# Kernel tuning notes

Measured on AMD Instinct MI355X. Metric: run time of the kernel, lower is better.

The kernel has to match this reference:

```python
import jax, jax.numpy as jnp
import numpy as np

B = 2048


def _maxpool2(x):
    return jax.lax.reduce_window(x, -jnp.inf, jax.lax.max,
                                 (1, 1, 2, 2), (1, 1, 2, 2), 'VALID')


def setup_inputs() -> dict:
    key = jax.random.key(0)
    ks = jax.random.split(key, 7)
    return {
        'x': jax.random.normal(ks[0], (B, 3, 32, 32), dtype=jnp.float32),
        'conv_w': jax.random.normal(ks[1], (45, 1, 5, 5), dtype=jnp.float32),
        'conv_b': jax.random.normal(ks[2], (45,), dtype=jnp.float32) * 0.1,
        'tree_w': jax.random.normal(ks[3], (1, 16, 15, 3, 7, 7, 2, 2), dtype=jnp.float32),
        'tree_b': jax.random.normal(ks[4], (1, 16, 3, 7), dtype=jnp.float32),
        'fc_w': jax.random.normal(ks[5], (10, 336), dtype=jnp.float32),
        'fc_b': jax.random.normal(ks[6], (10,), dtype=jnp.float32) * 0.1,
    }


def reference(x, conv_w, conv_b, tree_w, tree_b, fc_w, fc_b):
    # grouped conv: in=3, groups=3, out=45, kernel 5x5, VALID -> (B,45,28,28)
    out = jax.lax.conv_general_dilated(
        x, conv_w, window_strides=(1, 1), padding='VALID',
        dimension_numbers=('NCHW', 'OIHW', 'NCHW'), feature_group_count=3)
    out = jax.nn.sigmoid(out + conv_b[None, :, None, None])
    out = _maxpool2(out)  # (B,45,14,14)
    b = out.shape[0]
    # unfold((2,2),stride=2) + the torch reshape/transpose chain is equivalent to:
    # (B,45,14,14) -> (b, g=3, m=15, i=7, ki=2, j=7, kj=2) -> (b,m,g,i,j,ki,kj)
    xt = out.reshape(b, 3, 15, 7, 2, 7, 2).transpose(0, 2, 1, 3, 5, 4, 6)
    # TreeLayer: elementwise mul with weights (16,m,g,i,j,ki,kj) then sum over m,j,ki,kj
    t = jnp.einsum('bmgijkl,fmgijkl->bfgi', xt, tree_w[0]) + tree_b  # (B,16,3,7)
    t = jax.nn.sigmoid(t)
    return t.reshape(b, 16 * 3 * 7) @ fc_w.T + fc_b  # (B,10)
```

## Files before the change

kernel.cpp:

```cpp
#include <hip/hip_runtime.h>
#include <hip/hip_fp16.h>

#define BATCH 2048

typedef _Float16 f16x8 __attribute__((ext_vector_type(8)));
typedef float f32x4 __attribute__((ext_vector_type(4)));

#define RST 36
#define CST 1168
#define IMS 4672
#define IST 448
#define PIS 3152

__device__ __forceinline__ float fast_sigmoid(float v) {
    return __builtin_amdgcn_rcpf(1.0f + __builtin_amdgcn_exp2f(v * -1.44269504f));
}

#define WS_W3B  0
#define WS_FCW  301056

__global__ __launch_bounds__(256) void k_prep(
    const float* __restrict__ tree_w,
    const float* __restrict__ fc_w,
    ushort* __restrict__ W3B,
    float* __restrict__ FCW2,
    float* __restrict__ out)
{
    int pidx = blockIdx.x * 256 + threadIdx.x;
    if (pidx < 35280) {
        float4 v = ((const float4*)tree_w)[pidx];
        int j  = pidx % 7;
        int t1 = pidx / 7;
        int i  = t1 % 7;
        int t2 = t1 / 7;
        int g  = t2 % 3;
        int t3 = t2 / 3;
        int nn = t3 % 15;
        int f  = t3 / 15;
        int gi = g * 7 + i;
        int u  = nn & 7;
        int hi = nn >> 3;
        float vv[4] = {v.x, v.y, v.z, v.w};
        #pragma unroll
        for (int e = 0; e < 4; e++) {
            int ki = e >> 1, kj = e & 1;
            int u27 = ki * 14 + j * 2 + kj;
            int c   = u27 >> 1;
            int qq  = (u27 & 1) * 2 + hi;
            W3B[(size_t)(gi * 14 + c) * 512 + (qq * 16 + f) * 8 + u] =
                __half_as_ushort(__float2half(vv[e]));
        }
    } else if (pidx < 38640) {
        int jj = pidx - 35280;
        int f = jj & 15;
        int r = jj >> 4;
        int i = r % 7;
        int r2 = r / 7;
        int o = r2 % 10;
        int g = r2 / 10;
        FCW2[jj] = fc_w[o * 336 + f * 21 + g * 7 + i];
    } else if (pidx < 48048) {
        int z = pidx - 38640;
        int f  = z & 15;
        int qq = ((z >> 4) & 1) * 2 + 1;
        int r  = z >> 5;
        int c  = r % 14;
        int gi = r / 14;
        W3B[(size_t)(gi * 14 + c) * 512 + (qq * 16 + f) * 8 + 7] = 0;
    } else if (pidx < 68528) {
        out[pidx - 48048] = 0.f;
    }
}

__global__ __launch_bounds__(256, 3) void kF_all(
    const float* __restrict__ x,
    const float* __restrict__ conv_w,
    const float* __restrict__ conv_b,
    const ushort* __restrict__ W3B,
    const float* __restrict__ FCW2,
    const float* __restrict__ tree_b,
    const float* __restrict__ fc_b,
    float* __restrict__ out)
{
    __shared__ __align__(16) ushort xsc[2 * IMS];
    __shared__ __align__(16) ushort ps[4 * PIS];
    __shared__ __align__(16) ushort tsl[28 * 16];

    const int tid  = threadIdx.x;
    const int blk  = blockIdx.x;
    const int quad = blk / 3;
    const int g    = blk - quad * 3;
    const int img0 = quad * 4;
    const int lane = tid & 63;
    const int n    = lane & 15;
    const int q    = lane >> 4;
    const int wave = tid >> 6;

    float4 xv[4];
    #pragma unroll
    for (int im = 0; im < 4; im++)
        xv[im] = ((const float4*)(x + (size_t)(img0 + im) * 3072 + g * 1024))[tid];

    f16x8 B1 = {0, 0, 0, 0, 0, 0, 0, 0};
    f16x8 B2 = {0, 0, 0, 0, 0, 0, 0, 0};
    float bs = 0.f;
    if (n < 15) {
        const float* wrow = conv_w + (g * 15 + n) * 25;
        #pragma unroll
        for (int u = 0; u < 5; u++) B1[u] = (_Float16)wrow[q * 5 + u];
        if (q == 0) {
            #pragma unroll
            for (int u = 0; u < 5; u++) B2[u] = (_Float16)wrow[20 + u];
        }
        bs = conv_b[g * 15 + n] * -1.44269504f;
    }

    const int dr = (n >> 1) & 1, dc = n & 1, n4 = n >> 2;
    const int a2c = (4 - q) * RST;
    int aoff[13], svr[13];
    #pragma unroll
    for (int it = 0; it < 13; it++) {
        int t = wave + it * 4;
        int pb = t * 4 + n4;
        int ph = pb / 14, pw = pb - ph * 14;
        int r = 2 * ph + dr, c = 2 * pw + dc;
        int s = c & 3;
        aoff[it] = s * CST + (r + q) * RST + (c - s);
        int i = t / 7, tt = t - i * 7;
        svr[it] = i * IST + tt * 64 + lane;
    }

    auto conv_tile2 = [&](int it, ushort* pso) {
        const ushort* pA0 = xsc + aoff[it];
        const ushort* pA1 = pA0 + IMS;
        union U { struct { uint2 a, b; } u; f16x8 v; };
        U A1a, A2a, A1b, A2b;
        A1a.u.a = *(const uint2*)pA0;
        A1a.u.b = *(const uint2*)(pA0 + 4);
        A2a.u.a = *(const uint2*)(pA0 + a2c);
        A2a.u.b = *(const uint2*)(pA0 + a2c + 4);
        A1b.u.a = *(const uint2*)pA1;
        A1b.u.b = *(const uint2*)(pA1 + 4);
        A2b.u.a = *(const uint2*)(pA1 + a2c);
        A2b.u.b = *(const uint2*)(pA1 + a2c + 4);
        f32x4 da = {0.f, 0.f, 0.f, 0.f}, db = {0.f, 0.f, 0.f, 0.f};
        da = __builtin_amdgcn_mfma_f32_16x16x32_f16(A1a.v, B1, da, 0, 0, 0);
        db = __builtin_amdgcn_mfma_f32_16x16x32_f16(A1b.v, B1, db, 0, 0, 0);
        da = __builtin_amdgcn_mfma_f32_16x16x32_f16(A2a.v, B2, da, 0, 0, 0);
        db = __builtin_amdgcn_mfma_f32_16x16x32_f16(A2b.v, B2, db, 0, 0, 0);
        float mxa = fmaxf(fmaxf(da[0], da[1]), fmaxf(da[2], da[3]));
        float mxb = fmaxf(fmaxf(db[0], db[1]), fmaxf(db[2], db[3]));
        float ea = __builtin_amdgcn_exp2f(fmaf(mxa, -1.44269504f, bs));
        float eb = __builtin_amdgcn_exp2f(fmaf(mxb, -1.44269504f, bs));
        pso[svr[it]] =
            __half_as_ushort(__float2half(__builtin_amdgcn_rcpf(1.0f + ea)));
        pso[PIS + svr[it]] =
            __half_as_ushort(__float2half(__builtin_amdgcn_rcpf(1.0f + eb)));
    };

    const int row = tid >> 3, colg = (tid & 7) * 4;
    #pragma unroll
    for (int r2 = 0; r2 < 2; r2++) {
        #pragma unroll
        for (int im2 = 0; im2 < 2; im2++) {
            float4 v = xv[r2 * 2 + im2];
            __half2 a = __float22half2_rn(make_float2(v.x, v.y));
            __half2 b = __float22half2_rn(make_float2(v.z, v.w));
            unsigned d0 = *(unsigned*)&a, d1 = *(unsigned*)&b;
            unsigned n0 = (unsigned)__shfl_down((int)d0, 1);
            unsigned n1 = (unsigned)__shfl_down((int)d1, 1);
            if ((tid & 7) == 7) { n0 = 0u; n1 = 0u; }
            unsigned t01 = (d0 >> 16) | (d1 << 16);
            unsigned t12 = (d1 >> 16) | (n0 << 16);
            unsigned t23 = (n0 >> 16) | (n1 << 16);
            ushort* base = xsc + im2 * IMS + row * RST + colg;
            *(uint2*)(base)           = make_uint2(d0, d1);
            *(uint2*)(base + CST)     = make_uint2(t01, t12);
            *(uint2*)(base + 2 * CST) = make_uint2(d1, n0);
            *(uint2*)(base + 3 * CST) = make_uint2(t12, t23);
        }
        __syncthreads();

        ushort* pso = ps + (r2 * 2) * PIS;
        #pragma unroll
        for (int it = 0; it < 12; it++) conv_tile2(it, pso);
        if (wave == 0) conv_tile2(12, pso);
        __syncthreads();
    }

    for (int ii = wave; ii < 7; ii += 4) {
        const f16x8* Wb = (const f16x8*)W3B + (size_t)(g * 7 + ii) * 896;
        const ushort* ap = ps + (n & 3) * PIS + ii * IST;
        f16x8 Bf[14];
        #pragma unroll
        for (int c = 0; c < 14; c++) Bf[c] = Wb[c * 64 + lane];
        f32x4 D0 = {0.f, 0.f, 0.f, 0.f};
        f32x4 D1 = {0.f, 0.f, 0.f, 0.f};
        #pragma unroll
        for (int c = 0; c < 7; c++) {
            f16x8 Ae = *(const f16x8*)(ap + (2 * c) * 32 + q * 8);
            D0 = __builtin_amdgcn_mfma_f32_16x16x32_f16(Ae, Bf[2 * c], D0, 0, 0, 0);
            f16x8 Ao = *(const f16x8*)(ap + (2 * c + 1) * 32 + q * 8);
            D1 = __builtin_amdgcn_mfma_f32_16x16x32_f16(Ao, Bf[2 * c + 1], D1, 0, 0, 0);
        }
        if (q == 0) {
            float tb = tree_b[n * 21 + g * 7 + ii];
            #pragma unroll
            for (int im = 0; im < 4; im++) {
                float t = (D0[im] + D1[im]) + tb;
                tsl[(im * 7 + ii) * 16 + n] =
                    __half_as_ushort(__float2half(fast_sigmoid(t)));
            }
        }
    }
    __syncthreads();

    if (lane < 10) {
        const int im4 = wave, o = lane;
        const uint2* tp = (const uint2*)(tsl + im4 * 112);
        const float4* wp = (const float4*)(FCW2 + (size_t)(g * 10 + o) * 112);
        float acc = (g == 0) ? fc_b[o] : 0.f;
        #pragma unroll
        for (int jj = 0; jj < 28; jj++) {
            float4 w4 = wp[jj];
            uint2 hv = tp[jj];
            float2 p0 = __half22float2(*(const __half2*)&hv.x);
            float2 p1 = __half22float2(*(const __half2*)&hv.y);
            acc = fmaf(p0.x, w4.x, acc);
            acc = fmaf(p0.y, w4.y, acc);
            acc = fmaf(p1.x, w4.z, acc);
            acc = fmaf(p1.y, w4.w, acc);
        }
#if defined(__HIP_PLATFORM_AMD__)
        unsafeAtomicAdd(out + (size_t)(img0 + im4) * 10 + o, acc);
#else
        atomicAdd(out + (size_t)(img0 + im4) * 10 + o, acc);
#endif
    }
}

extern "C" void kernel_launch(void* const* d_in, const int* in_sizes, int n_in,
                              void* d_out, int out_size, void* d_ws, size_t ws_size,
                              hipStream_t stream) {
    const float* x      = (const float*)d_in[0];
    const float* conv_w = (const float*)d_in[1];
    const float* conv_b = (const float*)d_in[2];
    const float* tree_w = (const float*)d_in[3];
    const float* tree_b = (const float*)d_in[4];
    const float* fc_w   = (const float*)d_in[5];
    const float* fc_b   = (const float*)d_in[6];
    float* out = (float*)d_out;

    ushort* W3B  = (ushort*)((char*)d_ws + WS_W3B);
    float*  FCW2 = (float*)((char*)d_ws + WS_FCW);

    k_prep<<<268, 256, 0, stream>>>(tree_w, fc_w, W3B, FCW2, out);
    kF_all<<<512 * 3, 256, 0, stream>>>(x, conv_w, conv_b, W3B, FCW2,
                                        tree_b, fc_b, out);
}
```

Baseline: 110.8 us.

## Shrink shifted-image LDS layout to two word planes and raise occupancy

Replaces the four ushort column-shift planes of the staged fp16 image with two 32-bit-word planes (even/odd shift). This halves the LDS footprint and the pack-phase writes, and lets the conv A fragments be read as aligned dwords. Per-tile offsets are now computed incrementally instead of with divisions. The tree scratch buffer is aliased onto the image buffer, and launch bounds move from 3 to 4 blocks per CU to exploit the freed LDS. In exchange, A fragments are built from scalar dword loads instead of uint2 loads, and the tighter occupancy target may raise register pressure.

```diff
diff --git a/kernel.cpp b/kernel.cpp
--- a/kernel.cpp
+++ b/kernel.cpp
@@ -6,11 +6,10 @@
 typedef _Float16 f16x8 __attribute__((ext_vector_type(8)));
 typedef float f32x4 __attribute__((ext_vector_type(4)));
 
-#define RST 36
-#define CST 1168
-#define IMS 4672
-#define IST 448
-#define PIS 3152
+#define XROW 18
+#define XPL  584
+#define XIMG 1168
+#define PIS  3152
 
 __device__ __forceinline__ float fast_sigmoid(float v) {
     return __builtin_amdgcn_rcpf(1.0f + __builtin_amdgcn_exp2f(v * -1.44269504f));
@@ -72,7 +71,7 @@
     }
 }
 
-__global__ __launch_bounds__(256, 3) void kF_all(
+__global__ __launch_bounds__(256, 4) void kF_all(
     const float* __restrict__ x,
     const float* __restrict__ conv_w,
     const float* __restrict__ conv_b,
@@ -82,9 +81,9 @@
     const float* __restrict__ fc_b,
     float* __restrict__ out)
 {
-    __shared__ __align__(16) ushort xsc[2 * IMS];
+    __shared__ __align__(16) unsigned xsc[2 * XIMG];
     __shared__ __align__(16) ushort ps[4 * PIS];
-    __shared__ __align__(16) ushort tsl[28 * 16];
+    ushort* tsl = (ushort*)xsc;
 
     const int tid  = threadIdx.x;
     const int blk  = blockIdx.x;
@@ -101,6 +100,11 @@
     for (int im = 0; im < 4; im++)
         xv[im] = ((const float4*)(x + (size_t)(img0 + im) * 3072 + g * 1024))[tid];
 
+    if (tid < 128) {
+        int im = tid >> 6, pl = (tid >> 5) & 1, row = tid & 31;
+        *(uint2*)&xsc[im * XIMG + pl * XPL + row * XROW + 16] = make_uint2(0u, 0u);
+    }
+
     f16x8 B1 = {0, 0, 0, 0, 0, 0, 0, 0};
     f16x8 B2 = {0, 0, 0, 0, 0, 0, 0, 0};
     float bs = 0.f;
@@ -116,33 +120,47 @@
     }
 
     const int dr = (n >> 1) & 1, dc = n & 1, n4 = n >> 2;
-    const int a2c = (4 - q) * RST;
-    int aoff[13], svr[13];
-    #pragma unroll
-    for (int it = 0; it < 13; it++) {
-        int t = wave + it * 4;
-        int pb = t * 4 + n4;
-        int ph = pb / 14, pw = pb - ph * 14;
-        int r = 2 * ph + dr, c = 2 * pw + dc;
-        int s = c & 3;
-        aoff[it] = s * CST + (r + q) * RST + (c - s);
-        int i = t / 7, tt = t - i * 7;
-        svr[it] = i * IST + tt * 64 + lane;
-    }
+    const int a2cd = (4 - q) * XROW;
+    int aoffd[13];
+    {
+        int pb = wave * 4 + n4;
+        int ph = (pb >= 14) ? 1 : 0;
+        int pw = pb - 14 * ph;
+        int base = dc * XPL + (dr + q) * XROW;
+        #pragma unroll
+        for (int it = 0; it < 13; it++) {
+            aoffd[it] = base + 2 * ph * XROW + pw;
+            pw += 2; ph += 1;
+            if (pw >= 14) { pw -= 14; ph += 1; }
+        }
+    }
+
+    const int prow = tid >> 3, pt = tid & 7;
+    auto pack_img = [&](int im2, float4 v) {
+        __half2 a = __float22half2_rn(make_float2(v.x, v.y));
+        __half2 b = __float22half2_rn(make_float2(v.z, v.w));
+        unsigned d0 = *(unsigned*)&a, d1 = *(unsigned*)&b;
+        unsigned n0 = (unsigned)__shfl_down((int)d0, 1);
+        if (pt == 7) n0 = 0u;
+        unsigned t01 = (d0 >> 16) | (d1 << 16);
+        unsigned t12 = (d1 >> 16) | (n0 << 16);
+        unsigned* base = xsc + im2 * XIMG + prow * XROW + 2 * pt;
+        *(uint2*)(base)       = make_uint2(d0, d1);
+        *(uint2*)(base + XPL) = make_uint2(t01, t12);
+    };
 
     auto conv_tile2 = [&](int it, ushort* pso) {
-        const ushort* pA0 = xsc + aoff[it];
-        const ushort* pA1 = pA0 + IMS;
-        union U { struct { uint2 a, b; } u; f16x8 v; };
+        const unsigned* p0 = xsc + aoffd[it];
+        const unsigned* p1 = p0 + XIMG;
+        union U { unsigned w[4]; f16x8 v; };
         U A1a, A2a, A1b, A2b;
-        A1a.u.a = *(const uint2*)pA0;
-        A1a.u.b = *(const uint2*)(pA0 + 4);
-        A2a.u.a = *(const uint2*)(pA0 + a2c);
-        A2a.u.b = *(const uint2*)(pA0 + a2c + 4);
-        A1b.u.a = *(const uint2*)pA1;
-        A1b.u.b = *(const uint2*)(pA1 + 4);
-        A2b.u.a = *(const uint2*)(pA1 + a2c);
-        A2b.u.b = *(const uint2*)(pA1 + a2c + 4);
+        #pragma unroll
+        for (int e = 0; e < 4; e++) {
+            A1a.w[e] = p0[e];
+            A2a.w[e] = p0[a2cd + e];
+            A1b.w[e] = p1[e];
+            A2b.w[e] = p1[a2cd + e];
+        }
         f32x4 da = {0.f, 0.f, 0.f, 0.f}, db = {0.f, 0.f, 0.f, 0.f};
         da = __builtin_amdgcn_mfma_f32_16x16x32_f16(A1a.v, B1, da, 0, 0, 0);
         db = __builtin_amdgcn_mfma_f32_16x16x32_f16(A1b.v, B1, db, 0, 0, 0);
@@ -152,33 +170,17 @@
         float mxb = fmaxf(fmaxf(db[0], db[1]), fmaxf(db[2], db[3]));
         float ea = __builtin_amdgcn_exp2f(fmaf(mxa, -1.44269504f, bs));
         float eb = __builtin_amdgcn_exp2f(fmaf(mxb, -1.44269504f, bs));
-        pso[svr[it]] =
+        int so = (wave + it * 4) * 64 + lane;
+        pso[so] =
             __half_as_ushort(__float2half(__builtin_amdgcn_rcpf(1.0f + ea)));
-        pso[PIS + svr[it]] =
+        pso[PIS + so] =
             __half_as_ushort(__float2half(__builtin_amdgcn_rcpf(1.0f + eb)));
     };
 
-    const int row = tid >> 3, colg = (tid & 7) * 4;
     #pragma unroll
     for (int r2 = 0; r2 < 2; r2++) {
-        #pragma unroll
-        for (int im2 = 0; im2 < 2; im2++) {
-            float4 v = xv[r2 * 2 + im2];
-            __half2 a = __float22half2_rn(make_float2(v.x, v.y));
-            __half2 b = __float22half2_rn(make_float2(v.z, v.w));
-            unsigned d0 = *(unsigned*)&a, d1 = *(unsigned*)&b;
-            unsigned n0 = (unsigned)__shfl_down((int)d0, 1);
-            unsigned n1 = (unsigned)__shfl_down((int)d1, 1);
-            if ((tid & 7) == 7) { n0 = 0u; n1 = 0u; }
-            unsigned t01 = (d0 >> 16) | (d1 << 16);
-            unsigned t12 = (d1 >> 16) | (n0 << 16);
-            unsigned t23 = (n0 >> 16) | (n1 << 16);
-            ushort* base = xsc + im2 * IMS + row * RST + colg;
-            *(uint2*)(base)           = make_uint2(d0, d1);
-            *(uint2*)(base + CST)     = make_uint2(t01, t12);
-            *(uint2*)(base + 2 * CST) = make_uint2(d1, n0);
-            *(uint2*)(base + 3 * CST) = make_uint2(t12, t23);
-        }
+        pack_img(0, xv[r2 * 2 + 0]);
+        pack_img(1, xv[r2 * 2 + 1]);
         __syncthreads();
 
         ushort* pso = ps + (r2 * 2) * PIS;
@@ -190,7 +192,7 @@
 
     for (int ii = wave; ii < 7; ii += 4) {
         const f16x8* Wb = (const f16x8*)W3B + (size_t)(g * 7 + ii) * 896;
-        const ushort* ap = ps + (n & 3) * PIS + ii * IST;
+        const ushort* ap = ps + (n & 3) * PIS + ii * 448;
         f16x8 Bf[14];
         #pragma unroll
         for (int c = 0; c < 14; c++) Bf[c] = Wb[c * 64 + lane];
```

Result: faster. 102.3 us (-7.7%).
